# Kernel tuning notes

Measured on AMD Instinct MI355X. Metric: run time of the kernel, lower is better.

## Reference

```python
import jax, jax.numpy as jnp
import numpy as np

EMBED_DIM = 128
TEMP_DIM = EMBED_DIM // 4  # 32
NUM_TYPES = 50
DATE_SCALE = 1825.0
LN_EPS = 1e-5


def _layernorm(x, w, b):
    m = jnp.mean(x, axis=-1, keepdims=True)
    v = jnp.mean((x - m) ** 2, axis=-1, keepdims=True)
    return (x - m) * jax.lax.rsqrt(v + LN_EPS) * w + b


def setup_inputs() -> dict:
    key = jax.random.key(0)
    ks = jax.random.split(key, 16)
    B, L = 4096, 200
    inp = {
        "treatment_ids": jax.random.randint(ks[0], (B, L), 0, NUM_TYPES, dtype=jnp.int64 if jax.config.jax_enable_x64 else jnp.int32),
        "dates": jax.random.uniform(ks[1], (B, L), dtype=jnp.float32) * DATE_SCALE,
        "lengths": jax.random.randint(ks[2], (B,), 0, L + 1, dtype=jnp.int32),
        # parameters
        "emb": jax.random.normal(ks[3], (NUM_TYPES, EMBED_DIM), jnp.float32),
        "tp_w": jax.random.normal(ks[4], (1, TEMP_DIM), jnp.float32) * 0.1,
        "tp_b": jnp.zeros((TEMP_DIM,), jnp.float32),
        "tp_lnw": jnp.ones((TEMP_DIM,), jnp.float32),
        "tp_lnb": jnp.zeros((TEMP_DIM,), jnp.float32),
        "w1": jax.random.normal(ks[5], (EMBED_DIM + TEMP_DIM, EMBED_DIM), jnp.float32) * 0.05,
        "b1": jnp.zeros((EMBED_DIM,), jnp.float32),
        "ln1w": jnp.ones((EMBED_DIM,), jnp.float32),
        "ln1b": jnp.zeros((EMBED_DIM,), jnp.float32),
        "w2": jax.random.normal(ks[6], (EMBED_DIM, EMBED_DIM), jnp.float32) * 0.05,
        "b2": jnp.zeros((EMBED_DIM,), jnp.float32),
        "ln2w": jnp.ones((EMBED_DIM,), jnp.float32),
        "ln2b": jnp.zeros((EMBED_DIM,), jnp.float32),
    }
    return inp


def reference(treatment_ids, dates, lengths, emb, tp_w, tp_b, tp_lnw, tp_lnb,
              w1, b1, ln1w, ln1b, w2, b2, ln2w, ln2b):
    B, L = treatment_ids.shape
    mask = (jnp.arange(L)[None, :] < lengths[:, None]).astype(dates.dtype)  # [B, L]

    # embedding lookup [B, L, D]
    treat = emb[treatment_ids]

    # temporal projection: Linear(1 -> D/4) + LN + GELU
    dn = (dates / DATE_SCALE)[..., None]                      # [B, L, 1]
    temporal = dn * tp_w[0] + tp_b                            # [B, L, D/4]
    temporal = jax.nn.gelu(_layernorm(temporal, tp_lnw, tp_lnb), approximate=False)

    combined = jnp.concatenate([treat, temporal], axis=-1)    # [B, L, D + D/4]

    # sequence encoder (dropout is identity at eval)
    h = jnp.einsum("blk,kd->bld", combined, w1) + b1
    h = jax.nn.gelu(_layernorm(h, ln1w, ln1b), approximate=False)
    h = jnp.einsum("blk,kd->bld", h, w2) + b2
    h = _layernorm(h, ln2w, ln2b)                             # [B, L, D]

    # masked mean pool; empty histories -> zeros
    counts = jnp.sum(mask, axis=1, keepdims=True)             # [B, 1]
    pooled = jnp.sum(h * mask[..., None], axis=1) / jnp.maximum(counts, 1.0)
    return jnp.where(counts > 0, pooled, 0.0)                 # [B, D]
```

## Files before the change

### kernel.cpp

```cpp
#include <hip/hip_runtime.h>
#include <cmath>

#define LN_EPS 1e-5f

typedef float  f32x4  __attribute__((ext_vector_type(4)));
typedef float  f32x2  __attribute__((ext_vector_type(2)));
typedef short  short8 __attribute__((ext_vector_type(8)));
typedef unsigned int uint4v __attribute__((ext_vector_type(4)));

#define W1TF_U4 512
#define W2F_U4  2048
#define E1_U4   2450
#define WLDS_U4 2560

__device__ __forceinline__ unsigned short f32_bf16_rne(float f) {
    union { float f; unsigned u; } v; v.f = f;
    unsigned r = v.u + 0x7FFFu + ((v.u >> 16) & 1u);
    return (unsigned short)(r >> 16);
}

__device__ __forceinline__ unsigned cvt_pk_bf16(float lo, float hi) {
    unsigned r;
    asm("v_cvt_pk_bf16_f32 %0, %1, %2" : "=v"(r) : "v"(lo), "v"(hi));
    return r;
}

__device__ __forceinline__ float gelu_f(float x) {
    const float arg = x * fmaf(x * x, 0.044715f, 1.0f);
    const float e   = __builtin_amdgcn_exp2f(arg * -2.302258f);
    const float r   = __builtin_amdgcn_rcpf(e + 1.0f);
    return x * r;
}

template<int C>
__device__ __forceinline__ float dpp_radd(float x) {
    int t = __builtin_amdgcn_update_dpp(0, __builtin_bit_cast(int, x), C, 0xF, 0xF, true);
    return x + __builtin_bit_cast(float, t);
}
__device__ __forceinline__ float red16(float x) {
    x = dpp_radd<0x128>(x);
    x = dpp_radd<0x124>(x);
    x = dpp_radd<0x122>(x);
    x = dpp_radd<0x121>(x);
    return x;
}

__global__ void prep_kernel(const float* __restrict__ w1, const float* __restrict__ w2,
                            const float* __restrict__ emb, const float* __restrict__ b1,
                            const float* __restrict__ tp_w, const float* __restrict__ tp_b,
                            unsigned* __restrict__ ws) {
    const int tid = blockIdx.x * 256 + threadIdx.x;
    uint4v* w1tf = (uint4v*)ws;
    uint4v* w2f  = w1tf + W1TF_U4;
    float*  E1   = (float*)(w2f + W2F_U4);
    float*  tps  = E1 + 9800;

    for (int i = tid; i < W1TF_U4; i += 8192) {
        const int lane = i & 63, nt = i >> 6;
        const int k0 = 128 + (lane >> 4) * 8, n = nt * 16 + (lane & 15);
        uint4v r;
        #pragma unroll
        for (int j2 = 0; j2 < 4; ++j2) {
            unsigned lo = f32_bf16_rne(w1[(k0 + 2 * j2) * 128 + n]);
            unsigned hi = f32_bf16_rne(w1[(k0 + 2 * j2 + 1) * 128 + n]);
            r[j2] = lo | (hi << 16);
        }
        w1tf[i] = r;
    }
    for (int i = tid; i < W2F_U4; i += 8192) {
        const int lane = i & 63, nt = (i >> 6) & 7, kt = i >> 9;
        const int k0 = kt * 32 + (lane >> 4) * 8, n = nt * 16 + (lane & 15);
        uint4v r;
        #pragma unroll
        for (int j2 = 0; j2 < 4; ++j2) {
            unsigned lo = f32_bf16_rne(w2[(k0 + 2 * j2) * 128 + n]);
            unsigned hi = f32_bf16_rne(w2[(k0 + 2 * j2 + 1) * 128 + n]);
            r[j2] = lo | (hi << 16);
        }
        w2f[i] = r;
    }
    if (tid < 6400) {
        const int t = tid >> 7, n = tid & 127;
        float s = b1[n];
        #pragma unroll 4
        for (int k = 0; k < 128; ++k)
            s = fmaf(emb[t * 128 + k], w1[k * 128 + n], s);
        E1[t * 196 + (n & 15) * 12 + (n >> 4)] = s;
    }
    if (tid == 0) {
        float Sw = 0.f, Sb = 0.f, Sww = 0.f, Swb = 0.f, Sbb = 0.f;
        for (int j = 0; j < 32; ++j) {
            const float ww = tp_w[j], bb = tp_b[j];
            Sw += ww; Sb += bb; Sww += ww * ww; Swb += ww * bb; Sbb += bb * bb;
        }
        tps[0] = Sw; tps[1] = Sb; tps[2] = Sww; tps[3] = Swb; tps[4] = Sbb;
    }
}

__global__ __launch_bounds__(768, 3) void encoder_mfma(
    const int*   __restrict__ tids,  const float* __restrict__ dates,
    const int*   __restrict__ lengths,
    const float* __restrict__ tp_w,  const float* __restrict__ tp_b,
    const float* __restrict__ tp_lnw,const float* __restrict__ tp_lnb,
    const float* __restrict__ b1,    const float* __restrict__ ln1w, const float* __restrict__ ln1b,
    const float* __restrict__ b2,    const float* __restrict__ ln2w, const float* __restrict__ ln2b,
    const unsigned* __restrict__ ws, float* __restrict__ out,
    int B, int L)
{
    __shared__ __align__(16) uint4v wlds[WLDS_U4];
    __shared__ __align__(16) float  E1lds[9800];
    __shared__ __align__(16) unsigned short a2[12][4][64][8];
    __shared__ float poolbuf[3][12][128];
    __shared__ __align__(16) f32x4 tcoef[32];
    __shared__ __align__(16) f32x4 ecoef1[128];
    __shared__ __align__(8)  f32x2 ecoef2[128];

    const int tid = threadIdx.x;
    const int lane = tid & 63, w = tid >> 6;
    const int c = lane & 15, g = lane >> 4;
    const int b0 = blockIdx.x * 3;

    for (int i = tid; i < WLDS_U4; i += 768)
        wlds[i] = ((const uint4v*)ws)[i];
    for (int i = tid; i < E1_U4; i += 768)
        ((uint4v*)E1lds)[i] = ((const uint4v*)ws)[WLDS_U4 + i];

    const float* tps = (const float*)((const uint4v*)ws + WLDS_U4 + E1_U4);

    if (tid < 32)  tcoef[tid]  = (f32x4){tp_w[tid], tp_b[tid], tp_lnw[tid], tp_lnb[tid]};
    if (tid < 128) {
        ecoef1[tid] = (f32x4){0.f, ln1w[tid], ln1b[tid], 0.f};
        ecoef2[tid] = (f32x2){ln2w[tid], ln2b[tid]};
    }
    float b2c[8];
    #pragma unroll
    for (int nt = 0; nt < 8; ++nt) b2c[nt] = b2[nt * 16 + c];
    __syncthreads();

    const float Sw = tps[0], Sb = tps[1], Sww = tps[2], Swb = tps[3], Sbb = tps[4];

    const int len0 = (b0 + 0 < B) ? min(max(lengths[b0 + 0], 0), L) : 0;
    const int len1 = (b0 + 1 < B) ? min(max(lengths[b0 + 1], 0), L) : 0;
    const int len2 = (b0 + 2 < B) ? min(max(lengths[b0 + 2], 0), L) : 0;
    const int nt0 = (len0 + 15) >> 4, nt1 = (len1 + 15) >> 4, nt2 = (len2 + 15) >> 4;
    const int cum1 = nt0, cum2 = nt0 + nt1, T = cum2 + nt2;

    float pool0[8], pool1[8], pool2[8];
    #pragma unroll
    for (int nt = 0; nt < 8; ++nt) { pool0[nt] = 0.f; pool1[nt] = 0.f; pool2[nt] = 0.f; }
    const int srl = lane ^ ((lane >> 3) & 3);

    int pidr[4]; float pd = 0.f;
    if (w < T) {
        const int row0 = (w >= cum2) ? 2 : ((w >= cum1) ? 1 : 0);
        const int tl0  = w - ((row0 == 2) ? cum2 : ((row0 == 1) ? cum1 : 0));
        const long bs0 = (long)(b0 + row0) * L;
        const int R00  = tl0 << 4;
        pd = dates[bs0 + min(R00 + c, L - 1)] * (1.f / 1825.f);
        #pragma unroll
        for (int r = 0; r < 4; ++r)
            pidr[r] = tids[bs0 + min(R00 + 4 * g + r, L - 1)];
    }

    for (int t = w; t < T; t += 12) {
        const int row  = (t >= cum2) ? 2 : ((t >= cum1) ? 1 : 0);
        const int tl   = t - ((row == 2) ? cum2 : ((row == 1) ? cum1 : 0));
        const int lenr = (row == 2) ? len2 : ((row == 1) ? len1 : len0);
        const int R0   = tl << 4;

        int idr[4];
        #pragma unroll
        for (int r = 0; r < 4; ++r) idr[r] = pidr[r];
        const float d = pd;

        f32x4 acc[8];
        #pragma unroll
        for (int r = 0; r < 4; ++r) {
            const float* p = &E1lds[idr[r] * 196 + c * 12];
            const f32x4 lo = *(const f32x4*)p;
            const f32x4 hi = *(const f32x4*)(p + 4);
            acc[0][r] = lo[0]; acc[1][r] = lo[1]; acc[2][r] = lo[2]; acc[3][r] = lo[3];
            acc[4][r] = hi[0]; acc[5][r] = hi[1]; acc[6][r] = hi[2]; acc[7][r] = hi[3];
        }

        short8 tfrag;
        {
            const float tm = fmaf(d, Sw, Sb) * (1.f / 32.f);
            float tv = fmaf(d * d, Sww, fmaf(2.f * d, Swb, Sbb)) * (1.f / 32.f) - tm * tm;
            const float trs = rsqrtf(fmaxf(tv, 0.f) + LN_EPS);
            const int j0 = g * 8;
            uint4v r;
            #pragma unroll
            for (int j2 = 0; j2 < 4; ++j2) {
                const f32x4 t0 = tcoef[j0 + 2*j2];
                const f32x4 t1 = tcoef[j0 + 2*j2 + 1];
                const float y0 = fmaf((fmaf(d, t0[0], t0[1]) - tm) * trs, t0[2], t0[3]);
                const float y1 = fmaf((fmaf(d, t1[0], t1[1]) - tm) * trs, t1[2], t1[3]);
                r[j2] = cvt_pk_bf16(gelu_f(y0), gelu_f(y1));
            }
            union { uint4v u; short8 s; } cv; cv.u = r;
            tfrag = cv.s;
        }

        __builtin_amdgcn_s_setprio(1);
        #pragma unroll
        for (int nt = 0; nt < 8; ++nt) {
            const short8 bf = ((const short8*)wlds)[nt * 64 + lane];
            acc[nt] = __builtin_amdgcn_mfma_f32_16x16x32_bf16(tfrag, bf, acc[nt], 0, 0, 0);
        }
        __builtin_amdgcn_s_setprio(0);

        {
            const int tn = t + 12;
            if (tn < T) {
                const int rowN = (tn >= cum2) ? 2 : ((tn >= cum1) ? 1 : 0);
                const int tlN  = tn - ((rowN == 2) ? cum2 : ((rowN == 1) ? cum1 : 0));
                const long bsN = (long)(b0 + rowN) * L;
                const int R0N  = tlN << 4;
                pd = dates[bsN + min(R0N + c, L - 1)] * (1.f / 1825.f);
                #pragma unroll
                for (int r = 0; r < 4; ++r)
                    pidr[r] = tids[bsN + min(R0N + 4 * g + r, L - 1)];
            }
        }

        {
            f32x4 e1[8];
            #pragma unroll
            for (int nt = 0; nt < 8; ++nt) e1[nt] = ecoef1[nt * 16 + c];
            #pragma unroll
            for (int r = 0; r < 4; ++r) {
                float v[8], s = 0.f, q = 0.f;
                #pragma unroll
                for (int nt = 0; nt < 8; ++nt) {
                    v[nt] = acc[nt][r];
                    s += v[nt]; q = fmaf(v[nt], v[nt], q);
                }
                s = red16(s); q = red16(q);
                const float mean = s * (1.f / 128.f);
                const float var  = fmaxf(q * (1.f / 128.f) - mean * mean, 0.f);
                const float rstd = rsqrtf(var + LN_EPS);
                const int mrow = 4 * g + r;
                #pragma unroll
                for (int n2 = 0; n2 < 4; ++n2) {
                    const float y0 = gelu_f(fmaf((v[2*n2]   - mean) * rstd, e1[2*n2][1],   e1[2*n2][2]));
                    const float y1 = gelu_f(fmaf((v[2*n2+1] - mean) * rstd, e1[2*n2+1][1], e1[2*n2+1][2]));
                    const unsigned pk = cvt_pk_bf16(y0, y1);
                    {
                        const int kcol  = (2*n2) * 16 + c;
                        const int row64 = ((kcol >> 3) & 3) * 16 + mrow;
                        const int srow  = row64 ^ ((row64 >> 3) & 3);
                        a2[w][kcol >> 5][srow][kcol & 7] = (unsigned short)(pk & 0xffffu);
                    }
                    {
                        const int kcol  = (2*n2+1) * 16 + c;
                        const int row64 = ((kcol >> 3) & 3) * 16 + mrow;
                        const int srow  = row64 ^ ((row64 >> 3) & 3);
                        a2[w][kcol >> 5][srow][kcol & 7] = (unsigned short)(pk >> 16);
                    }
                }
            }
        }

        asm volatile("" ::: "memory");

        f32x4 acc2[8];
        #pragma unroll
        for (int nt = 0; nt < 8; ++nt)
            acc2[nt] = (f32x4){b2c[nt], b2c[nt], b2c[nt], b2c[nt]};
        __builtin_amdgcn_s_setprio(1);
        #pragma unroll
        for (int kt2 = 0; kt2 < 4; ++kt2) {
            short8 af;
            __builtin_memcpy(&af, &a2[w][kt2][srl][0], 16);
            #pragma unroll
            for (int nt = 0; nt < 8; ++nt) {
                const short8 bf = ((const short8*)(wlds + W1TF_U4))[(kt2 * 8 + nt) * 64 + lane];
                acc2[nt] = __builtin_amdgcn_mfma_f32_16x16x32_bf16(af, bf, acc2[nt], 0, 0, 0);
            }
        }
        __builtin_amdgcn_s_setprio(0);

        asm volatile("" ::: "memory");

        {
            float A[8], Sbv = 0.f, Sgv = 0.f;
            #pragma unroll
            for (int nt = 0; nt < 8; ++nt) A[nt] = 0.f;
            #pragma unroll
            for (int r = 0; r < 4; ++r) {
                float s = 0.f, q = 0.f;
                #pragma unroll
                for (int nt = 0; nt < 8; ++nt) {
                    const float v = acc2[nt][r];
                    s += v; q = fmaf(v, v, q);
                }
                s = red16(s); q = red16(q);
                const float mean = s * (1.f / 128.f);
                const float var  = fmaxf(q * (1.f / 128.f) - mean * mean, 0.f);
                const float rstd = rsqrtf(var + LN_EPS);
                const float msk  = ((R0 + 4 * g + r) < lenr) ? 1.f : 0.f;
                const float alf  = msk * rstd;
                Sbv = fmaf(alf, mean, Sbv);
                Sgv += msk;
                #pragma unroll
                for (int nt = 0; nt < 8; ++nt)
                    A[nt] = fmaf(acc2[nt][r], alf, A[nt]);
            }
            if (row == 0) {
                #pragma unroll
                for (int nt = 0; nt < 8; ++nt) {
                    const f32x2 e = ecoef2[nt * 16 + c];
                    pool0[nt] = fmaf(e[0], A[nt] - Sbv, fmaf(e[1], Sgv, pool0[nt]));
                }
            } else if (row == 1) {
                #pragma unroll
                for (int nt = 0; nt < 8; ++nt) {
                    const f32x2 e = ecoef2[nt * 16 + c];
                    pool1[nt] = fmaf(e[0], A[nt] - Sbv, fmaf(e[1], Sgv, pool1[nt]));
                }
            } else {
                #pragma unroll
                for (int nt = 0; nt < 8; ++nt) {
                    const f32x2 e = ecoef2[nt * 16 + c];
                    pool2[nt] = fmaf(e[0], A[nt] - Sbv, fmaf(e[1], Sgv, pool2[nt]));
                }
            }
        }
    }

    #pragma unroll
    for (int nt = 0; nt < 8; ++nt) {
        float t0 = pool0[nt]; t0 += __shfl_xor(t0, 16); t0 += __shfl_xor(t0, 32); pool0[nt] = t0;
        float t1 = pool1[nt]; t1 += __shfl_xor(t1, 16); t1 += __shfl_xor(t1, 32); pool1[nt] = t1;
        float t2 = pool2[nt]; t2 += __shfl_xor(t2, 16); t2 += __shfl_xor(t2, 32); pool2[nt] = t2;
    }
    if (g == 0) {
        #pragma unroll
        for (int nt = 0; nt < 8; ++nt) {
            poolbuf[0][w][nt * 16 + c] = pool0[nt];
            poolbuf[1][w][nt * 16 + c] = pool1[nt];
            poolbuf[2][w][nt * 16 + c] = pool2[nt];
        }
    }
    __syncthreads();
    if (tid < 384) {
        const int r3  = tid >> 7;
        const int col = tid & 127;
        const int bo  = b0 + r3;
        if (bo < B) {
            const int lenb = min(max(lengths[bo], 0), L);
            float s = 0.f;
            #pragma unroll
            for (int k = 0; k < 12; ++k) s += poolbuf[r3][k][col];
            out[bo * 128 + col] = (lenb > 0) ? s / (float)lenb : 0.f;
        }
    }
}

extern "C" void kernel_launch(void* const* d_in, const int* in_sizes, int n_in,
                              void* d_out, int out_size, void* d_ws, size_t ws_size,
                              hipStream_t stream) {
    const int*   tids    = (const int*)  d_in[0];
    const float* dates   = (const float*)d_in[1];
    const int*   lengths = (const int*)  d_in[2];
    const float* emb     = (const float*)d_in[3];
    const float* tp_w    = (const float*)d_in[4];
    const float* tp_b    = (const float*)d_in[5];
    const float* tp_lnw  = (const float*)d_in[6];
    const float* tp_lnb  = (const float*)d_in[7];
    const float* w1      = (const float*)d_in[8];
    const float* b1      = (const float*)d_in[9];
    const float* ln1w    = (const float*)d_in[10];
    const float* ln1b    = (const float*)d_in[11];
    const float* w2      = (const float*)d_in[12];
    const float* b2      = (const float*)d_in[13];
    const float* ln2w    = (const float*)d_in[14];
    const float* ln2b    = (const float*)d_in[15];
    float* out = (float*)d_out;

    const int B = in_sizes[2];
    const int L = in_sizes[0] / B;

    hipLaunchKernelGGL(prep_kernel, dim3(32), dim3(256), 0, stream,
                       w1, w2, emb, b1, tp_w, tp_b, (unsigned*)d_ws);
    hipLaunchKernelGGL(encoder_mfma, dim3((B + 2) / 3), dim3(768), 0, stream,
                       tids, dates, lengths, tp_w, tp_b, tp_lnw, tp_lnb,
                       b1, ln1w, ln1b, b2, ln2w, ln2b,
                       (const unsigned*)d_ws, out, B, L);
}
```

Before: 191.1 us.

## Process six batch rows per block with LDS atomic pooling

Each 768-thread block now handles six batch rows instead of three, so the roughly 40KB+ LDS weight and E1 staging is spread over twice as much work and the grid is halved. Per-row register pool accumulators are replaced by per-tile cross-lane reductions followed by LDS atomicAdd into a six-row pool buffer, which removes the row-dependent branching and register pressure. The prep kernel is also launched with more blocks. The change adds LDS atomic traffic per tile and a longer tile-location chain, and fewer blocks may reduce load balance across CUs.

After: 197.6 us. +3.4%, slower.

```diff
diff --git a/kernel.cpp b/kernel.cpp
--- a/kernel.cpp
+++ b/kernel.cpp
@@ -50,12 +50,13 @@
                             const float* __restrict__ tp_w, const float* __restrict__ tp_b,
                             unsigned* __restrict__ ws) {
     const int tid = blockIdx.x * 256 + threadIdx.x;
+    const int NT  = 65536;
     uint4v* w1tf = (uint4v*)ws;
     uint4v* w2f  = w1tf + W1TF_U4;
     float*  E1   = (float*)(w2f + W2F_U4);
     float*  tps  = E1 + 9800;
 
-    for (int i = tid; i < W1TF_U4; i += 8192) {
+    for (int i = tid; i < W1TF_U4; i += NT) {
         const int lane = i & 63, nt = i >> 6;
         const int k0 = 128 + (lane >> 4) * 8, n = nt * 16 + (lane & 15);
         uint4v r;
@@ -67,7 +68,7 @@
         }
         w1tf[i] = r;
     }
-    for (int i = tid; i < W2F_U4; i += 8192) {
+    for (int i = tid; i < W2F_U4; i += NT) {
         const int lane = i & 63, nt = (i >> 6) & 7, kt = i >> 9;
         const int k0 = kt * 32 + (lane >> 4) * 8, n = nt * 16 + (lane & 15);
         uint4v r;
@@ -110,7 +111,7 @@
     __shared__ __align__(16) uint4v wlds[WLDS_U4];
     __shared__ __align__(16) float  E1lds[9800];
     __shared__ __align__(16) unsigned short a2[12][4][64][8];
-    __shared__ float poolbuf[3][12][128];
+    __shared__ float poolrow[6][128];
     __shared__ __align__(16) f32x4 tcoef[32];
     __shared__ __align__(16) f32x4 ecoef1[128];
     __shared__ __align__(8)  f32x2 ecoef2[128];
@@ -118,12 +119,13 @@
     const int tid = threadIdx.x;
     const int lane = tid & 63, w = tid >> 6;
     const int c = lane & 15, g = lane >> 4;
-    const int b0 = blockIdx.x * 3;
+    const int b0 = blockIdx.x * 6;
 
     for (int i = tid; i < WLDS_U4; i += 768)
         wlds[i] = ((const uint4v*)ws)[i];
     for (int i = tid; i < E1_U4; i += 768)
         ((uint4v*)E1lds)[i] = ((const uint4v*)ws)[WLDS_U4 + i];
+    poolrow[tid >> 7][tid & 127] = 0.f;
 
     const float* tps = (const float*)((const uint4v*)ws + WLDS_U4 + E1_U4);
 
@@ -139,21 +141,32 @@
 
     const float Sw = tps[0], Sb = tps[1], Sww = tps[2], Swb = tps[3], Sbb = tps[4];
 
-    const int len0 = (b0 + 0 < B) ? min(max(lengths[b0 + 0], 0), L) : 0;
-    const int len1 = (b0 + 1 < B) ? min(max(lengths[b0 + 1], 0), L) : 0;
-    const int len2 = (b0 + 2 < B) ? min(max(lengths[b0 + 2], 0), L) : 0;
-    const int nt0 = (len0 + 15) >> 4, nt1 = (len1 + 15) >> 4, nt2 = (len2 + 15) >> 4;
-    const int cum1 = nt0, cum2 = nt0 + nt1, T = cum2 + nt2;
-
-    float pool0[8], pool1[8], pool2[8];
+    int lenA[6];
     #pragma unroll
-    for (int nt = 0; nt < 8; ++nt) { pool0[nt] = 0.f; pool1[nt] = 0.f; pool2[nt] = 0.f; }
+    for (int i = 0; i < 6; ++i)
+        lenA[i] = (b0 + i < B) ? min(max(lengths[b0 + i], 0), L) : 0;
+    const int m0 = (lenA[0] + 15) >> 4, m1 = (lenA[1] + 15) >> 4, m2 = (lenA[2] + 15) >> 4;
+    const int m3 = (lenA[3] + 15) >> 4, m4 = (lenA[4] + 15) >> 4, m5 = (lenA[5] + 15) >> 4;
+    const int cum1 = m0, cum2 = cum1 + m1, cum3 = cum2 + m2;
+    const int cum4 = cum3 + m3, cum5 = cum4 + m4, T = cum5 + m5;
+    const int len0 = lenA[0], len1 = lenA[1], len2 = lenA[2];
+    const int len3 = lenA[3], len4 = lenA[4], len5 = lenA[5];
+
+    auto locate = [&](int t, int& row, int& tl, int& lenr) {
+        if      (t >= cum5) { row = 5; tl = t - cum5; lenr = len5; }
+        else if (t >= cum4) { row = 4; tl = t - cum4; lenr = len4; }
+        else if (t >= cum3) { row = 3; tl = t - cum3; lenr = len3; }
+        else if (t >= cum2) { row = 2; tl = t - cum2; lenr = len2; }
+        else if (t >= cum1) { row = 1; tl = t - cum1; lenr = len1; }
+        else                { row = 0; tl = t;        lenr = len0; }
+    };
+
     const int srl = lane ^ ((lane >> 3) & 3);
 
     int pidr[4]; float pd = 0.f;
     if (w < T) {
-        const int row0 = (w >= cum2) ? 2 : ((w >= cum1) ? 1 : 0);
-        const int tl0  = w - ((row0 == 2) ? cum2 : ((row0 == 1) ? cum1 : 0));
+        int row0, tl0, lx;
+        locate(w, row0, tl0, lx);
         const long bs0 = (long)(b0 + row0) * L;
         const int R00  = tl0 << 4;
         pd = dates[bs0 + min(R00 + c, L - 1)] * (1.f / 1825.f);
@@ -163,10 +176,9 @@
     }
 
     for (int t = w; t < T; t += 12) {
-        const int row  = (t >= cum2) ? 2 : ((t >= cum1) ? 1 : 0);
-        const int tl   = t - ((row == 2) ? cum2 : ((row == 1) ? cum1 : 0));
-        const int lenr = (row == 2) ? len2 : ((row == 1) ? len1 : len0);
-        const int R0   = tl << 4;
+        int row, tl, lenr;
+        locate(t, row, tl, lenr);
+        const int R0 = tl << 4;
 
         int idr[4];
         #pragma unroll
@@ -213,8 +225,8 @@
         {
             const int tn = t + 12;
             if (tn < T) {
-                const int rowN = (tn >= cum2) ? 2 : ((tn >= cum1) ? 1 : 0);
-                const int tlN  = tn - ((rowN == 2) ? cum2 : ((rowN == 1) ? cum1 : 0));
+                int rowN, tlN, lx;
+                locate(tn, rowN, tlN, lx);
                 const long bsN = (long)(b0 + rowN) * L;
                 const int R0N  = tlN << 4;
                 pd = dates[bsN + min(R0N + c, L - 1)] * (1.f / 1825.f);
@@ -307,53 +319,31 @@
                 for (int nt = 0; nt < 8; ++nt)
                     A[nt] = fmaf(acc2[nt][r], alf, A[nt]);
             }
-            if (row == 0) {
-                #pragma unroll
-                for (int nt = 0; nt < 8; ++nt) {
-                    const f32x2 e = ecoef2[nt * 16 + c];
-                    pool0[nt] = fmaf(e[0], A[nt] - Sbv, fmaf(e[1], Sgv, pool0[nt]));
-                }
-            } else if (row == 1) {
-                #pragma unroll
-                for (int nt = 0; nt < 8; ++nt) {
-                    const f32x2 e = ecoef2[nt * 16 + c];
-                    pool1[nt] = fmaf(e[0], A[nt] - Sbv, fmaf(e[1], Sgv, pool1[nt]));
-                }
-            } else {
-                #pragma unroll
-                for (int nt = 0; nt < 8; ++nt) {
-                    const f32x2 e = ecoef2[nt * 16 + c];
-                    pool2[nt] = fmaf(e[0], A[nt] - Sbv, fmaf(e[1], Sgv, pool2[nt]));
-                }
-            }
-        }
-    }
-
-    #pragma unroll
-    for (int nt = 0; nt < 8; ++nt) {
-        float t0 = pool0[nt]; t0 += __shfl_xor(t0, 16); t0 += __shfl_xor(t0, 32); pool0[nt] = t0;
-        float t1 = pool1[nt]; t1 += __shfl_xor(t1, 16); t1 += __shfl_xor(t1, 32); pool1[nt] = t1;
-        float t2 = pool2[nt]; t2 += __shfl_xor(t2, 16); t2 += __shfl_xor(t2, 32); pool2[nt] = t2;
-    }
-    if (g == 0) {
-        #pragma unroll
-        for (int nt = 0; nt < 8; ++nt) {
-            poolbuf[0][w][nt * 16 + c] = pool0[nt];
-            poolbuf[1][w][nt * 16 + c] = pool1[nt];
-            poolbuf[2][w][nt * 16 + c] = pool2[nt];
-        }
-    }
+            float ptile[8];
+            #pragma unroll
+            for (int nt = 0; nt < 8; ++nt) {
+                const f32x2 e = ecoef2[nt * 16 + c];
+                float tv = fmaf(e[0], A[nt] - Sbv, e[1] * Sgv);
+                tv += __shfl_xor(tv, 16);
+                tv += __shfl_xor(tv, 32);
+                ptile[nt] = tv;
+            }
+            if (g == 0) {
+                #pragma unroll
+                for (int nt = 0; nt < 8; ++nt)
+                    atomicAdd(&poolrow[row][nt * 16 + c], ptile[nt]);
+            }
+        }
+    }
+
     __syncthreads();
-    if (tid < 384) {
-        const int r3  = tid >> 7;
+    {
+        const int r6  = tid >> 7;
         const int col = tid & 127;
-        const int bo  = b0 + r3;
+        const int bo  = b0 + r6;
         if (bo < B) {
             const int lenb = min(max(lengths[bo], 0), L);
-            float s = 0.f;
-            #pragma unroll
-            for (int k = 0; k < 12; ++k) s += poolbuf[r3][k][col];
-            out[bo * 128 + col] = (lenb > 0) ? s / (float)lenb : 0.f;
+            out[bo * 128 + col] = (lenb > 0) ? poolrow[r6][col] / (float)lenb : 0.f;
         }
     }
 }
@@ -382,9 +372,9 @@
     const int B = in_sizes[2];
     const int L = in_sizes[0] / B;
 
-    hipLaunchKernelGGL(prep_kernel, dim3(32), dim3(256), 0, stream,
+    hipLaunchKernelGGL(prep_kernel, dim3(256), dim3(256), 0, stream,
                        w1, w2, emb, b1, tp_w, tp_b, (unsigned*)d_ws);
-    hipLaunchKernelGGL(encoder_mfma, dim3((B + 2) / 3), dim3(768), 0, stream,
+    hipLaunchKernelGGL(encoder_mfma, dim3((B + 5) / 6), dim3(768), 0, stream,
                        tids, dates, lengths, tp_w, tp_b, tp_lnw, tp_lnb,
                        b1, ln1w, ln1b, b2, ln2w, ln2b,
                        (const unsigned*)d_ws, out, B, L);
```
